# Kernel optimization log

Measured on AMD Instinct MI355X. Metric: run time of the kernel, lower is better.

The kernel has to match this reference:

```python
import jax, jax.numpy as jnp
import numpy as np

N_TOKENS = 4096
EMBED = 1024
ATTN = 64


def setup_inputs() -> dict:
    key = jax.random.key(0)
    k1, k2, k3, k4 = jax.random.split(key, 4)
    tokens = jax.random.normal(k1, (N_TOKENS, EMBED), dtype=jnp.float32)
    mask = jnp.ones((1, N_TOKENS), dtype=jnp.float32)
    W_Q = jax.random.uniform(k2, (EMBED, ATTN), dtype=jnp.float32)
    W_K = jax.random.uniform(k3, (EMBED, ATTN), dtype=jnp.float32)
    W_V = jax.random.uniform(k4, (EMBED, ATTN), dtype=jnp.float32)
    return {"tokens": tokens, "mask": mask, "W_Q": W_Q, "W_K": W_K, "W_V": W_V}


def reference(tokens, mask, W_Q, W_K, W_V):
    # Q, K, V: (n_tokens, attn)
    Q = tokens @ W_Q
    K = tokens @ W_K
    V = tokens @ W_V
    scale = jnp.sqrt(jnp.asarray(ATTN, dtype=tokens.dtype))
    # scores: (n_tokens, n_tokens); multiplicative mask then scale, as in source
    scores = (Q @ K.T) * mask
    attn = jax.nn.softmax(scores / scale, axis=1)
    return attn @ V
```

## Files before the change

### kernel.cpp

```cpp
#include <hip/hip_runtime.h>
#include <math.h>

#define NT 4096
#define EMB 1024
#define DH 64
#define PLANE (NT * DH)
#define NSPLIT 16
#define KPS (NT / NSPLIT)
#define KVB 64
#define KSPLIT 8
#define LOG2E 1.44269504088896f

typedef __attribute__((ext_vector_type(8))) short short8;
typedef __attribute__((ext_vector_type(16))) float f32x16;
typedef unsigned short u16;

union U8 { short8 s; uint4 u; unsigned short h[8]; unsigned int w[4]; };

static __device__ __forceinline__ unsigned short f2bf(float x) {
    union { float f; unsigned int u; } v; v.f = x;
    unsigned int r = v.u + 0x7fffu + ((v.u >> 16) & 1u);
    return (unsigned short)(r >> 16);
}
static __device__ __forceinline__ float bf2f(unsigned short h) {
    union { unsigned int u; float f; } v; v.u = ((unsigned int)h) << 16;
    return v.f;
}
static __device__ __forceinline__ unsigned int cvtpk(float a, float b) {
    unsigned int r;
    asm("v_cvt_pk_bf16_f32 %0, %1, %2" : "=v"(r) : "v"(a), "v"(b));
    return r;
}
static __device__ __forceinline__ void split2(float a, float b,
                                              unsigned int& h, unsigned int& lo) {
    h = cvtpk(a, b);
    union { unsigned int u; float f; } ua, ub;
    ua.u = h << 16;
    ub.u = h & 0xffff0000u;
    lo = cvtpk(a - ua.f, b - ub.f);
}

__global__ __launch_bounds__(256) void proj_mfma(
    const float* __restrict__ tokens,
    const float* __restrict__ wq, const float* __restrict__ wk,
    const float* __restrict__ wv,
    float* __restrict__ part)
{
    __shared__ u16 Th[128][64];
    __shared__ u16 Tl[128][64];
    __shared__ u16 Wh[96][64];
    __shared__ u16 Wl[96][64];

    const int t  = threadIdx.x;
    const int rb = blockIdx.x;
    const int cb = blockIdx.y;
    const int ks = blockIdx.z;
    const int w    = t >> 6;
    const int lane = t & 63;
    const int g    = lane >> 5;
    const int c    = lane & 31;
    const int rowbase = rb * 128;

    f32x16 acc[3];
#pragma unroll
    for (int ct = 0; ct < 3; ++ct)
#pragma unroll
        for (int i = 0; i < 16; ++i) acc[ct][i] = 0.f;

    for (int st = 0; st < 2; ++st) {
        const int kbase = ks * (EMB / KSPLIT) + st * 64;
        __syncthreads();
#pragma unroll
        for (int i = 0; i < 4; ++i) {
            int idx = t + 256 * i;
            int r = idx >> 3;
            int slot = idx & 7;
            const float* gp = tokens + (size_t)(rowbase + r) * EMB + kbase + slot * 8;
            float4 a = *(const float4*)gp;
            float4 b = *(const float4*)(gp + 4);
            uint4 H, L;
            split2(a.x, a.y, H.x, L.x);
            split2(a.z, a.w, H.y, L.y);
            split2(b.x, b.y, H.z, L.z);
            split2(b.z, b.w, H.w, L.w);
            int dst = (slot ^ (r & 7)) * 8;
            *(uint4*)&Th[r][dst] = H;
            *(uint4*)&Tl[r][dst] = L;
        }
#pragma unroll
        for (int i = 0; i < 3; ++i) {
            int idx = t + 256 * i;
            int col = idx >> 3;
            int slot = idx & 7;
            int colg = cb * 96 + col;
            const float* W = (colg < 64) ? wq : (colg < 128) ? wk : wv;
            const float* wp = W + (size_t)(kbase + slot * 8) * DH + (colg & 63);
            float x[8];
#pragma unroll
            for (int j = 0; j < 8; ++j) x[j] = wp[j * DH];
            uint4 H, L;
            split2(x[0], x[1], H.x, L.x);
            split2(x[2], x[3], H.y, L.y);
            split2(x[4], x[5], H.z, L.z);
            split2(x[6], x[7], H.w, L.w);
            int dst = (slot ^ (col & 7)) * 8;
            *(uint4*)&Wh[col][dst] = H;
            *(uint4*)&Wl[col][dst] = L;
        }
        __syncthreads();

#pragma unroll
        for (int kt = 0; kt < 4; ++kt) {
            int sA = kt * 2 + g;
            int offA = ((sA ^ (c & 7)) * 8);
            short8 ah = *(const short8*)&Th[w * 32 + c][offA];
            short8 al = *(const short8*)&Tl[w * 32 + c][offA];
#pragma unroll
            for (int ct = 0; ct < 3; ++ct) {
                short8 bh = *(const short8*)&Wh[ct * 32 + c][offA];
                short8 bl = *(const short8*)&Wl[ct * 32 + c][offA];
                acc[ct] = __builtin_amdgcn_mfma_f32_32x32x16_bf16(ah, bh, acc[ct], 0, 0, 0);
                acc[ct] = __builtin_amdgcn_mfma_f32_32x32x16_bf16(ah, bl, acc[ct], 0, 0, 0);
                acc[ct] = __builtin_amdgcn_mfma_f32_32x32x16_bf16(al, bh, acc[ct], 0, 0, 0);
            }
        }
    }

#pragma unroll
    for (int ct = 0; ct < 3; ++ct)
#pragma unroll
        for (int r = 0; r < 16; ++r) {
            int row_l = (r & 3) + 8 * (r >> 2) + 4 * g;
            part[((size_t)ks * NT + rowbase + w * 32 + row_l) * 192 + cb * 96 + ct * 32 + c]
                = acc[ct][r];
        }
}

__global__ __launch_bounds__(256) void merge_conv(
    const float* __restrict__ part, const float* __restrict__ mask,
    u16* __restrict__ Qhg, u16* __restrict__ Qlg,
    u16* __restrict__ Khg, u16* __restrict__ Klg, u16* __restrict__ Vbg)
{
    int tid = blockIdx.x * 256 + threadIdx.x;
    int row = tid / 24;
    int c8  = tid % 24;
    int colbase = c8 * 8;

    float v[8];
#pragma unroll
    for (int i = 0; i < 8; ++i) v[i] = 0.f;
#pragma unroll
    for (int s = 0; s < KSPLIT; ++s) {
        const float* p = part + ((size_t)s * NT + row) * 192 + colbase;
        float4 a = *(const float4*)p;
        float4 b = *(const float4*)(p + 4);
        v[0] += a.x; v[1] += a.y; v[2] += a.z; v[3] += a.w;
        v[4] += b.x; v[5] += b.y; v[6] += b.z; v[7] += b.w;
    }

    int plane = colbase >> 6;
    int pc = colbase & 63;
    size_t o = (size_t)row * DH + pc;
    if (plane == 0) {
        uint4 H, L;
        split2(v[0], v[1], H.x, L.x);
        split2(v[2], v[3], H.y, L.y);
        split2(v[4], v[5], H.z, L.z);
        split2(v[6], v[7], H.w, L.w);
        *(uint4*)&Qhg[o] = H;
        *(uint4*)&Qlg[o] = L;
    } else if (plane == 1) {
        float mk = mask[row] * 0.125f * LOG2E;
        uint4 H, L;
        split2(v[0] * mk, v[1] * mk, H.x, L.x);
        split2(v[2] * mk, v[3] * mk, H.y, L.y);
        split2(v[4] * mk, v[5] * mk, H.z, L.z);
        split2(v[6] * mk, v[7] * mk, H.w, L.w);
        *(uint4*)&Khg[o] = H;
        *(uint4*)&Klg[o] = L;
    } else {
        uint4 H;
        H.x = cvtpk(v[0], v[1]);
        H.y = cvtpk(v[2], v[3]);
        H.z = cvtpk(v[4], v[5]);
        H.w = cvtpk(v[6], v[7]);
        *(uint4*)&Vbg[o] = H;
    }
}

__global__ __launch_bounds__(256) void attn_mfma(
    const u16* __restrict__ Qhg, const u16* __restrict__ Qlg,
    const u16* __restrict__ Khg, const u16* __restrict__ Klg,
    const u16* __restrict__ Vbg,
    u16* __restrict__ opart, float* __restrict__ mlbuf)
{
    __shared__ u16 Kh[2][64][64];
    __shared__ u16 Kl[2][64][64];
    __shared__ unsigned int V2[2][32][64];

    const int t    = threadIdx.x;
    const int qb   = blockIdx.x;
    const int sp   = blockIdx.y;
    const int wq   = t >> 6;
    const int lane = t & 63;
    const int g    = lane >> 5;
    const int c    = lane & 31;
    const int qrow = qb * 128 + wq * 32 + c;

    auto stage = [&](int b, int kv) {
#pragma unroll
        for (int it = 0; it < 2; ++it) {
            int idx = it * 256 + t;
            int j = idx >> 3, gr = idx & 7;
            int colp = (gr * 8) ^ ((j & 7) * 8);
            *(uint4*)&Kh[b][j][colp] = *(const uint4*)&Khg[(size_t)(kv + j) * DH + gr * 8];
            *(uint4*)&Kl[b][j][colp] = *(const uint4*)&Klg[(size_t)(kv + j) * DH + gr * 8];
        }
        {
            int a2 = t >> 3, dg = t & 7;
            uint4 r0 = *(const uint4*)&Vbg[(size_t)(kv + a2 * 2) * DH + dg * 8];
            uint4 r1 = *(const uint4*)&Vbg[(size_t)(kv + a2 * 2 + 1) * DH + dg * 8];
            const unsigned int* p0 = (const unsigned int*)&r0;
            const unsigned int* p1 = (const unsigned int*)&r1;
            unsigned int wv_[8];
#pragma unroll
            for (int i = 0; i < 4; ++i) {
                wv_[2 * i]     = (p0[i] & 0xFFFFu) | (p1[i] << 16);
                wv_[2 * i + 1] = (p0[i] >> 16)     | (p1[i] & 0xFFFF0000u);
            }
            int colp = (dg * 8) ^ ((a2 & 7) * 8);
            *(uint4*)&V2[b][a2][colp]     = *(uint4*)&wv_[0];
            *(uint4*)&V2[b][a2][colp + 4] = *(uint4*)&wv_[4];
        }
    };

    short8 qh[4], ql[4];
#pragma unroll
    for (int kt = 0; kt < 4; ++kt) {
        size_t o = (size_t)qrow * DH + kt * 16 + g * 8;
        U8 H, L;
        H.u = *(const uint4*)&Qhg[o];
        L.u = *(const uint4*)&Qlg[o];
        qh[kt] = H.s;
        ql[kt] = L.s;
    }

    f32x16 oa[2];
#pragma unroll
    for (int i = 0; i < 16; ++i) { oa[0][i] = 0.f; oa[1][i] = 0.f; }
    float m = -INFINITY, l = 0.f;

    stage(0, sp * KPS);
    __syncthreads();

    for (int cb = 0; cb < KPS / KVB; ++cb) {
        const int cur = cb & 1;
        if (cb + 1 < KPS / KVB) stage(cur ^ 1, sp * KPS + (cb + 1) * KVB);

        f32x16 st0, st1;
#pragma unroll
        for (int i = 0; i < 16; ++i) { st0[i] = 0.f; st1[i] = 0.f; }
#pragma unroll
        for (int kt = 0; kt < 4; ++kt) {
            int colp = ((kt * 2 + g) * 8) ^ ((c & 7) * 8);
            short8 kh0 = *(const short8*)&Kh[cur][c][colp];
            short8 kl0 = *(const short8*)&Kl[cur][c][colp];
            short8 kh1 = *(const short8*)&Kh[cur][32 + c][colp];
            short8 kl1 = *(const short8*)&Kl[cur][32 + c][colp];
            st0 = __builtin_amdgcn_mfma_f32_32x32x16_bf16(kh0, qh[kt], st0, 0, 0, 0);
            st1 = __builtin_amdgcn_mfma_f32_32x32x16_bf16(kh1, qh[kt], st1, 0, 0, 0);
            st0 = __builtin_amdgcn_mfma_f32_32x32x16_bf16(kh0, ql[kt], st0, 0, 0, 0);
            st1 = __builtin_amdgcn_mfma_f32_32x32x16_bf16(kh1, ql[kt], st1, 0, 0, 0);
            st0 = __builtin_amdgcn_mfma_f32_32x32x16_bf16(kl0, qh[kt], st0, 0, 0, 0);
            st1 = __builtin_amdgcn_mfma_f32_32x32x16_bf16(kl1, qh[kt], st1, 0, 0, 0);
        }

        float p[32];
        float pm = -INFINITY;
#pragma unroll
        for (int r = 0; r < 16; ++r) {
            pm = fmaxf(pm, st0[r]);
            pm = fmaxf(pm, st1[r]);
        }
        pm = fmaxf(pm, __shfl_xor(pm, 32));
        float mn = fmaxf(m, pm);
        float f  = exp2f(m - mn);
        float rs = 0.f;
#pragma unroll
        for (int r = 0; r < 16; ++r) { p[r]      = exp2f(st0[r] - mn); rs += p[r]; }
#pragma unroll
        for (int r = 0; r < 16; ++r) { p[16 + r] = exp2f(st1[r] - mn); rs += p[16 + r]; }
        rs += __shfl_xor(rs, 32);
        l = l * f + rs;
        m = mn;

        short8 pa[4];
#pragma unroll
        for (int jt = 0; jt < 2; ++jt) {
            const float* pp = &p[jt * 16];
            unsigned int A1 = cvtpk(pp[0], pp[1]),   B1 = cvtpk(pp[4], pp[5]);
            unsigned int A2 = cvtpk(pp[2], pp[3]),   B2 = cvtpk(pp[6], pp[7]);
            unsigned int A3 = cvtpk(pp[8], pp[9]),   B3 = cvtpk(pp[12], pp[13]);
            unsigned int A4 = cvtpk(pp[10], pp[11]), B4 = cvtpk(pp[14], pp[15]);
            unsigned int xA1 = (unsigned int)__shfl_xor((int)A1, 32);
            unsigned int xB1 = (unsigned int)__shfl_xor((int)B1, 32);
            unsigned int xA2 = (unsigned int)__shfl_xor((int)A2, 32);
            unsigned int xB2 = (unsigned int)__shfl_xor((int)B2, 32);
            unsigned int xA3 = (unsigned int)__shfl_xor((int)A3, 32);
            unsigned int xB3 = (unsigned int)__shfl_xor((int)B3, 32);
            unsigned int xA4 = (unsigned int)__shfl_xor((int)A4, 32);
            unsigned int xB4 = (unsigned int)__shfl_xor((int)B4, 32);
            U8 f0, f1;
            f0.w[0] = g ? xB1 : A1;
            f0.w[1] = g ? xB2 : A2;
            f0.w[2] = g ? B1  : xA1;
            f0.w[3] = g ? B2  : xA2;
            f1.w[0] = g ? xB3 : A3;
            f1.w[1] = g ? xB4 : A4;
            f1.w[2] = g ? B3  : xA3;
            f1.w[3] = g ? B4  : xA4;
            pa[jt * 2]     = f0.s;
            pa[jt * 2 + 1] = f1.s;
        }

#pragma unroll
        for (int r = 0; r < 16; ++r) {
            float fr = __shfl(f, (r & 3) + 8 * (r >> 2) + 4 * g);
            oa[0][r] *= fr;
            oa[1][r] *= fr;
        }

#pragma unroll
        for (int dt = 0; dt < 2; ++dt) {
#pragma unroll
            for (int ksl = 0; ksl < 4; ++ksl) {
                U8 bf;
#pragma unroll
                for (int pq = 0; pq < 4; ++pq) {
                    int j2 = ksl * 8 + g * 4 + pq;
                    int col = (dt * 32 + c) ^ ((j2 & 7) * 8);
                    bf.w[pq] = V2[cur][j2][col];
                }
                oa[dt] = __builtin_amdgcn_mfma_f32_32x32x16_bf16(pa[ksl], bf.s, oa[dt], 0, 0, 0);
            }
        }
        __syncthreads();
    }

    float inv = 1.f / l;
#pragma unroll
    for (int r = 0; r < 16; ++r) {
        int crow = (r & 3) + 8 * (r >> 2) + 4 * g;
        float li = __shfl(inv, crow);
        int row = qb * 128 + wq * 32 + crow;
        size_t o = ((size_t)sp * NT + row) * DH + c;
        opart[o]      = f2bf(oa[0][r] * li);
        opart[o + 32] = f2bf(oa[1][r] * li);
    }
    if (lane < 32) {
        int row = qb * 128 + wq * 32 + lane;
        mlbuf[((size_t)sp * NT + row) * 2 + 0] = m;
        mlbuf[((size_t)sp * NT + row) * 2 + 1] = l;
    }
}

__global__ __launch_bounds__(256) void merge_kernel(
    const u16* __restrict__ opart, const float* __restrict__ mlbuf,
    float* __restrict__ out)
{
    int idx = (blockIdx.x * 256 + threadIdx.x) * 4;
    int row = idx >> 6;
    int d0  = idx & 63;

    float mv[NSPLIT], lv[NSPLIT];
    float mstar = -INFINITY;
#pragma unroll
    for (int s = 0; s < NSPLIT; ++s) {
        mv[s] = mlbuf[((size_t)s * NT + row) * 2 + 0];
        lv[s] = mlbuf[((size_t)s * NT + row) * 2 + 1];
        mstar = fmaxf(mstar, mv[s]);
    }
    float denom = 0.f;
    float ax = 0.f, ay = 0.f, az = 0.f, aw = 0.f;
#pragma unroll
    for (int s = 0; s < NSPLIT; ++s) {
        float w = lv[s] * exp2f(mv[s] - mstar);
        denom += w;
        uint2 ov = *(const uint2*)&opart[((size_t)s * NT + row) * DH + d0];
        ax += w * bf2f((u16)(ov.x & 0xFFFFu));
        ay += w * bf2f((u16)(ov.x >> 16));
        az += w * bf2f((u16)(ov.y & 0xFFFFu));
        aw += w * bf2f((u16)(ov.y >> 16));
    }
    float inv = 1.f / denom;
    *(float4*)&out[idx] = make_float4(ax * inv, ay * inv, az * inv, aw * inv);
}

extern "C" void kernel_launch(void* const* d_in, const int* in_sizes, int n_in,
                              void* d_out, int out_size, void* d_ws, size_t ws_size,
                              hipStream_t stream) {
    const float* tokens = (const float*)d_in[0];
    const float* mask   = (const float*)d_in[1];
    const float* wq     = (const float*)d_in[2];
    const float* wk     = (const float*)d_in[3];
    const float* wv     = (const float*)d_in[4];
    char*  wsb = (char*)d_ws;
    float* out = (float*)d_out;

    u16* Qhg  = (u16*)wsb;
    u16* Qlg  = Qhg + PLANE;
    u16* Khg  = Qlg + PLANE;
    u16* Klg  = Khg + PLANE;
    u16* Vbg  = Klg + PLANE;
    float* part  = (float*)(wsb + (size_t)4 * 1024 * 1024);
    u16*   opart = (u16*)(wsb + (size_t)4 * 1024 * 1024);
    float* mlbuf = (float*)(wsb + (size_t)28 * 1024 * 1024);

    hipLaunchKernelGGL(proj_mfma, dim3(32, 2, KSPLIT), dim3(256), 0, stream,
                       tokens, wq, wk, wv, part);
    hipLaunchKernelGGL(merge_conv, dim3(384), dim3(256), 0, stream,
                       part, mask, Qhg, Qlg, Khg, Klg, Vbg);
    hipLaunchKernelGGL(attn_mfma, dim3(NT / 128, NSPLIT), dim3(256), 0, stream,
                       Qhg, Qlg, Khg, Klg, Vbg, opart, mlbuf);
    hipLaunchKernelGGL(merge_kernel, dim3(256), dim3(256), 0, stream,
                       opart, mlbuf, out);
}
```

Before: 50.21 us.

## Double KV tile to 128, drop double buffering, cap launch bounds at two blocks

The KV tile per iteration grows from 64 to 128 keys and the double-buffered shared-memory staging is replaced by a single buffer loaded between two barriers. Launch bounds now request 2 blocks per SM. The aim is fewer loop iterations and softmax/rescale passes per key, and higher occupancy so other blocks can hide the loads that are no longer prefetched. The cost is that global loads are exposed inside each block, and the larger register footprint (64 score floats, 8 P fragments) may spill under the occupancy cap.

```diff
diff --git a/kernel.cpp b/kernel.cpp
--- a/kernel.cpp
+++ b/kernel.cpp
@@ -7,7 +7,7 @@
 #define PLANE (NT * DH)
 #define NSPLIT 16
 #define KPS (NT / NSPLIT)
-#define KVB 64
+#define KVB 128
 #define KSPLIT 8
 #define LOG2E 1.44269504088896f
 
@@ -188,15 +188,15 @@
     }
 }
 
-__global__ __launch_bounds__(256) void attn_mfma(
+__global__ __launch_bounds__(256, 2) void attn_mfma(
     const u16* __restrict__ Qhg, const u16* __restrict__ Qlg,
     const u16* __restrict__ Khg, const u16* __restrict__ Klg,
     const u16* __restrict__ Vbg,
     u16* __restrict__ opart, float* __restrict__ mlbuf)
 {
-    __shared__ u16 Kh[2][64][64];
-    __shared__ u16 Kl[2][64][64];
-    __shared__ unsigned int V2[2][32][64];
+    __shared__ u16 Kh[128][64];
+    __shared__ u16 Kl[128][64];
+    __shared__ unsigned int V2[64][64];
 
     const int t    = threadIdx.x;
     const int qb   = blockIdx.x;
@@ -207,33 +207,6 @@
     const int c    = lane & 31;
     const int qrow = qb * 128 + wq * 32 + c;
 
-    auto stage = [&](int b, int kv) {
-#pragma unroll
-        for (int it = 0; it < 2; ++it) {
-            int idx = it * 256 + t;
-            int j = idx >> 3, gr = idx & 7;
-            int colp = (gr * 8) ^ ((j & 7) * 8);
-            *(uint4*)&Kh[b][j][colp] = *(const uint4*)&Khg[(size_t)(kv + j) * DH + gr * 8];
-            *(uint4*)&Kl[b][j][colp] = *(const uint4*)&Klg[(size_t)(kv + j) * DH + gr * 8];
-        }
-        {
-            int a2 = t >> 3, dg = t & 7;
-            uint4 r0 = *(const uint4*)&Vbg[(size_t)(kv + a2 * 2) * DH + dg * 8];
-            uint4 r1 = *(const uint4*)&Vbg[(size_t)(kv + a2 * 2 + 1) * DH + dg * 8];
-            const unsigned int* p0 = (const unsigned int*)&r0;
-            const unsigned int* p1 = (const unsigned int*)&r1;
-            unsigned int wv_[8];
-#pragma unroll
-            for (int i = 0; i < 4; ++i) {
-                wv_[2 * i]     = (p0[i] & 0xFFFFu) | (p1[i] << 16);
-                wv_[2 * i + 1] = (p0[i] >> 16)     | (p1[i] & 0xFFFF0000u);
-            }
-            int colp = (dg * 8) ^ ((a2 & 7) * 8);
-            *(uint4*)&V2[b][a2][colp]     = *(uint4*)&wv_[0];
-            *(uint4*)&V2[b][a2][colp + 4] = *(uint4*)&wv_[4];
-        }
-    };
-
     short8 qh[4], ql[4];
 #pragma unroll
     for (int kt = 0; kt < 4; ++kt) {
@@ -250,53 +223,79 @@
     for (int i = 0; i < 16; ++i) { oa[0][i] = 0.f; oa[1][i] = 0.f; }
     float m = -INFINITY, l = 0.f;
 
-    stage(0, sp * KPS);
-    __syncthreads();
-
     for (int cb = 0; cb < KPS / KVB; ++cb) {
-        const int cur = cb & 1;
-        if (cb + 1 < KPS / KVB) stage(cur ^ 1, sp * KPS + (cb + 1) * KVB);
-
-        f32x16 st0, st1;
-#pragma unroll
-        for (int i = 0; i < 16; ++i) { st0[i] = 0.f; st1[i] = 0.f; }
+        const int kv = sp * KPS + cb * KVB;
+        __syncthreads();
+#pragma unroll
+        for (int it = 0; it < 4; ++it) {
+            int idx = it * 256 + t;
+            int j = idx >> 3, gr = idx & 7;
+            int colp = (gr * 8) ^ ((j & 7) * 8);
+            *(uint4*)&Kh[j][colp] = *(const uint4*)&Khg[(size_t)(kv + j) * DH + gr * 8];
+            *(uint4*)&Kl[j][colp] = *(const uint4*)&Klg[(size_t)(kv + j) * DH + gr * 8];
+        }
+#pragma unroll
+        for (int it = 0; it < 2; ++it) {
+            int idx = it * 256 + t;
+            int a2 = idx >> 3, dg = idx & 7;
+            uint4 r0 = *(const uint4*)&Vbg[(size_t)(kv + a2 * 2) * DH + dg * 8];
+            uint4 r1 = *(const uint4*)&Vbg[(size_t)(kv + a2 * 2 + 1) * DH + dg * 8];
+            const unsigned int* p0 = (const unsigned int*)&r0;
+            const unsigned int* p1 = (const unsigned int*)&r1;
+            unsigned int wv_[8];
+#pragma unroll
+            for (int i = 0; i < 4; ++i) {
+                wv_[2 * i]     = (p0[i] & 0xFFFFu) | (p1[i] << 16);
+                wv_[2 * i + 1] = (p0[i] >> 16)     | (p1[i] & 0xFFFF0000u);
+            }
+            int colp = (dg * 8) ^ ((a2 & 7) * 8);
+            *(uint4*)&V2[a2][colp]     = *(uint4*)&wv_[0];
+            *(uint4*)&V2[a2][colp + 4] = *(uint4*)&wv_[4];
+        }
+        __syncthreads();
+
+        f32x16 st[4];
+#pragma unroll
+        for (int jt = 0; jt < 4; ++jt)
+#pragma unroll
+            for (int i = 0; i < 16; ++i) st[jt][i] = 0.f;
 #pragma unroll
         for (int kt = 0; kt < 4; ++kt) {
             int colp = ((kt * 2 + g) * 8) ^ ((c & 7) * 8);
-            short8 kh0 = *(const short8*)&Kh[cur][c][colp];
-            short8 kl0 = *(const short8*)&Kl[cur][c][colp];
-            short8 kh1 = *(const short8*)&Kh[cur][32 + c][colp];
-            short8 kl1 = *(const short8*)&Kl[cur][32 + c][colp];
-            st0 = __builtin_amdgcn_mfma_f32_32x32x16_bf16(kh0, qh[kt], st0, 0, 0, 0);
-            st1 = __builtin_amdgcn_mfma_f32_32x32x16_bf16(kh1, qh[kt], st1, 0, 0, 0);
-            st0 = __builtin_amdgcn_mfma_f32_32x32x16_bf16(kh0, ql[kt], st0, 0, 0, 0);
-            st1 = __builtin_amdgcn_mfma_f32_32x32x16_bf16(kh1, ql[kt], st1, 0, 0, 0);
-            st0 = __builtin_amdgcn_mfma_f32_32x32x16_bf16(kl0, qh[kt], st0, 0, 0, 0);
-            st1 = __builtin_amdgcn_mfma_f32_32x32x16_bf16(kl1, qh[kt], st1, 0, 0, 0);
-        }
-
-        float p[32];
+#pragma unroll
+            for (int jt = 0; jt < 4; ++jt) {
+                short8 kh = *(const short8*)&Kh[jt * 32 + c][colp];
+                short8 kl = *(const short8*)&Kl[jt * 32 + c][colp];
+                st[jt] = __builtin_amdgcn_mfma_f32_32x32x16_bf16(kh, qh[kt], st[jt], 0, 0, 0);
+                st[jt] = __builtin_amdgcn_mfma_f32_32x32x16_bf16(kh, ql[kt], st[jt], 0, 0, 0);
+                st[jt] = __builtin_amdgcn_mfma_f32_32x32x16_bf16(kl, qh[kt], st[jt], 0, 0, 0);
+            }
+        }
+
+        float p[64];
         float pm = -INFINITY;
 #pragma unroll
-        for (int r = 0; r < 16; ++r) {
-            pm = fmaxf(pm, st0[r]);
-            pm = fmaxf(pm, st1[r]);
-        }
+        for (int jt = 0; jt < 4; ++jt)
+#pragma unroll
+            for (int r = 0; r < 16; ++r) pm = fmaxf(pm, st[jt][r]);
         pm = fmaxf(pm, __shfl_xor(pm, 32));
         float mn = fmaxf(m, pm);
         float f  = exp2f(m - mn);
         float rs = 0.f;
 #pragma unroll
-        for (int r = 0; r < 16; ++r) { p[r]      = exp2f(st0[r] - mn); rs += p[r]; }
-#pragma unroll
-        for (int r = 0; r < 16; ++r) { p[16 + r] = exp2f(st1[r] - mn); rs += p[16 + r]; }
+        for (int jt = 0; jt < 4; ++jt)
+#pragma unroll
+            for (int r = 0; r < 16; ++r) {
+                p[jt * 16 + r] = exp2f(st[jt][r] - mn);
+                rs += p[jt * 16 + r];
+            }
         rs += __shfl_xor(rs, 32);
         l = l * f + rs;
         m = mn;
 
-        short8 pa[4];
-#pragma unroll
-        for (int jt = 0; jt < 2; ++jt) {
+        short8 pa[8];
+#pragma unroll
+        for (int jt = 0; jt < 4; ++jt) {
             const float* pp = &p[jt * 16];
             unsigned int A1 = cvtpk(pp[0], pp[1]),   B1 = cvtpk(pp[4], pp[5]);
             unsigned int A2 = cvtpk(pp[2], pp[3]),   B2 = cvtpk(pp[6], pp[7]);
@@ -333,18 +332,17 @@
 #pragma unroll
         for (int dt = 0; dt < 2; ++dt) {
 #pragma unroll
-            for (int ksl = 0; ksl < 4; ++ksl) {
+            for (int ksl = 0; ksl < 8; ++ksl) {
                 U8 bf;
 #pragma unroll
                 for (int pq = 0; pq < 4; ++pq) {
                     int j2 = ksl * 8 + g * 4 + pq;
                     int col = (dt * 32 + c) ^ ((j2 & 7) * 8);
-                    bf.w[pq] = V2[cur][j2][col];
+                    bf.w[pq] = V2[j2][col];
                 }
                 oa[dt] = __builtin_amdgcn_mfma_f32_32x32x16_bf16(pa[ksl], bf.s, oa[dt], 0, 0, 0);
             }
         }
-        __syncthreads();
     }
 
     float inv = 1.f / l;
```

Measured after the change: 48.50 us, median of 2. 3.4% less time.
